# Kernel optimization log

Hardware: AMD Instinct MI355X
Metric: run time of the kernel (lower is better)

The kernel has to match this reference:

```python
import jax, jax.numpy as jnp
import numpy as np

FS = 5  # filter_size


def _extract_patches(x, fs):
    """x: (B, C, H, W) -> (B, C, fs*fs, H, W), 'same' padding, row-major
    shift order matching conv2d with an identity (one-hot) kernel."""
    B, C, H, W = x.shape
    pad = fs // 2
    xp = jnp.pad(x, ((0, 0), (0, 0), (pad, pad), (pad, pad)))
    shifts = [xp[:, :, i:i + H, j:j + W] for i in range(fs) for j in range(fs)]
    return jnp.stack(shifts, axis=2)


def setup_inputs() -> dict:
    key = jax.random.key(0)
    k1, k2 = jax.random.split(key)
    B, C, H, W = 8, 32, 128, 128
    x = jax.random.normal(k1, (B, C, H, W), dtype=jnp.float32)
    # PPDFGen modeled as a per-pixel linear map C -> fs^2 (1x1 conv) + bias
    w_gen = jax.random.normal(k2, (FS * FS, C), dtype=jnp.float32) * (1.0 / np.sqrt(C))
    b_gen = jnp.zeros((FS * FS,), dtype=jnp.float32)
    return {"x": x, "w_gen": w_gen, "b_gen": b_gen}


def reference(x, w_gen, b_gen):
    # Per-pixel dynamic filters: (B, fs^2, H, W)
    filters = jnp.einsum('bchw,fc->bfhw', x, w_gen) + b_gen[None, :, None, None]
    # Shifted patches (im2col via identity-kernel conv in the original):
    patches = _extract_patches(x, FS)            # (B, C, fs^2, H, W)
    # Elementwise multiply by filters (broadcast over channels) and reduce
    # over the fs^2 tap axis -- same math as the per-channel loop + concat.
    out = jnp.einsum('bcfhw,bfhw->bchw', patches, filters)
    return out
```

## Files before the change

### kernel.cpp

```cpp
#include <hip/hip_runtime.h>

#define FS    5
#define NTAP  25
#define Bc    8
#define Cc    32
#define Hc    128
#define Wc    128
#define HW    (Hc * Wc)

#define TH      8
#define TW      64
#define HALO_H  12
#define HALO_W  72
#define PLANE   (HALO_H * HALO_W)
#define LDS_FLOATS (Cc * PLANE)
#define LDS_BYTES  (LDS_FLOATS * 4)
#define F4_PER_PLANE (PLANE / 4)
#define F4_TOTAL     (Cc * F4_PER_PLANE)
#define INSTR_TOTAL  (F4_TOTAL / 64)
#define NWAVE        4
#define INSTR_PER_WAVE (INSTR_TOTAL / NWAVE)

__device__ __attribute__((aligned(16))) float ZERO4[4];

__device__ __forceinline__ void gload_lds16(const float* g, float* lds) {
    __builtin_amdgcn_global_load_lds(
        (const __attribute__((address_space(1))) void*)g,
        (__attribute__((address_space(3))) void*)lds, 16, 0, 0);
}

__global__ __launch_bounds__(256, 1) void ppdfn_fused(
    const float* __restrict__ x, const float* __restrict__ wg,
    const float* __restrict__ bg, float* __restrict__ out)
{
    extern __shared__ float xs[];

    const int tid  = threadIdx.x;
    const int lane = tid & 63;
    const int wv   = tid >> 6;
    const int ht   = blockIdx.x;
    const int wt   = blockIdx.y;
    const int b    = blockIdx.z;
    const int h0   = ht * TH;
    const int w0   = wt * TW;

    const float* xb = x + (size_t)b * Cc * HW;

    const int f_base = wv * (INSTR_PER_WAVE * 64) + lane;
#pragma unroll
    for (int k = 0; k < INSTR_PER_WAVE; ++k) {
        const int f  = f_base + k * 64;
        const int c  = f / F4_PER_PLANE;
        const int rm = f - c * F4_PER_PLANE;
        const int r  = rm / 18;
        const int c4 = rm - r * 18;
        const int gh = h0 - 2 + r;
        const int gw = w0 - 4 + 4 * c4;
        const bool v = ((unsigned)gh < (unsigned)Hc) &&
                       ((unsigned)gw <= (unsigned)(Wc - 4));
        const float* src = v ? (xb + (size_t)c * HW + gh * Wc + gw) : ZERO4;
        gload_lds16(src, xs + (size_t)(wv * INSTR_PER_WAVE + k) * 256);
    }
    asm volatile("s_waitcnt vmcnt(0)" ::: "memory");
    __syncthreads();

    const int ty = tid >> 5;
    const int tx = tid & 31;
    const int w2 = tx * 2;

    float fx[NTAP], fy[NTAP];
#pragma unroll
    for (int t = 0; t < NTAP; ++t) { const float bv = bg[t]; fx[t] = bv; fy[t] = bv; }

#pragma unroll 4
    for (int c = 0; c < Cc; ++c) {
        const float2 xv = *reinterpret_cast<const float2*>(
            xs + c * PLANE + (ty + 2) * HALO_W + (w2 + 4));
#pragma unroll
        for (int t = 0; t < NTAP; ++t) {
            const float wv_ = wg[t * Cc + c];
            fx[t] = fmaf(wv_, xv.x, fx[t]);
            fy[t] = fmaf(wv_, xv.y, fy[t]);
        }
    }

    float* ob = out + (size_t)b * Cc * HW + (h0 + ty) * Wc + (w0 + w2);
#pragma unroll 2
    for (int c = 0; c < Cc; ++c) {
        const float* p = xs + c * PLANE + ty * HALO_W + (w2 + 2);
        float ax = 0.f, ay = 0.f;
#pragma unroll
        for (int di = 0; di < FS; ++di) {
            const float* row = p + di * HALO_W;
            const float2 s01 = *reinterpret_cast<const float2*>(row);
            const float2 s23 = *reinterpret_cast<const float2*>(row + 2);
            const float2 s45 = *reinterpret_cast<const float2*>(row + 4);
            const float s0 = s01.x, s1 = s01.y, s2 = s23.x,
                        s3 = s23.y, s4 = s45.x, s5 = s45.y;
            ax = fmaf(fx[di * FS + 0], s0, ax);  ay = fmaf(fy[di * FS + 0], s1, ay);
            ax = fmaf(fx[di * FS + 1], s1, ax);  ay = fmaf(fy[di * FS + 1], s2, ay);
            ax = fmaf(fx[di * FS + 2], s2, ax);  ay = fmaf(fy[di * FS + 2], s3, ay);
            ax = fmaf(fx[di * FS + 3], s3, ax);  ay = fmaf(fy[di * FS + 3], s4, ay);
            ax = fmaf(fx[di * FS + 4], s4, ax);  ay = fmaf(fy[di * FS + 4], s5, ay);
        }
        *reinterpret_cast<float2*>(ob + (size_t)c * HW) = make_float2(ax, ay);
    }
}

extern "C" void kernel_launch(void* const* d_in, const int* in_sizes, int n_in,
                              void* d_out, int out_size, void* d_ws, size_t ws_size,
                              hipStream_t stream) {
    const float* x  = (const float*)d_in[0];
    const float* wg = (const float*)d_in[1];
    const float* bg = (const float*)d_in[2];
    float* out = (float*)d_out;

    ppdfn_fused<<<dim3(Hc / TH, Wc / TW, Bc), 256, LDS_BYTES, stream>>>(
        x, wg, bg, out);
}
```

Baseline: 23.24 us.

## Split channels across blocks, recomputing filters from directly loaded center pixels

Each block now handles only an 8-channel group, so it stages an 8-channel halo tile in LDS instead of all 32 channels. This cuts LDS per block and allows 4 blocks per CU, with 1024 blocks instead of 256. The per-pixel filters still need all 32 channels, so each block loads the other 24 channels' center pixels straight from global memory into registers, double-buffered to overlap with the FMAs. The cost is that filter generation is repeated four times per tile and there is extra global traffic for the center pixels.

```diff
diff --git a/kernel.cpp b/kernel.cpp
--- a/kernel.cpp
+++ b/kernel.cpp
@@ -4,6 +4,7 @@
 #define NTAP  25
 #define Bc    8
 #define Cc    32
+#define CG    8
 #define Hc    128
 #define Wc    128
 #define HW    (Hc * Wc)
@@ -13,13 +14,9 @@
 #define HALO_H  12
 #define HALO_W  72
 #define PLANE   (HALO_H * HALO_W)
-#define LDS_FLOATS (Cc * PLANE)
-#define LDS_BYTES  (LDS_FLOATS * 4)
 #define F4_PER_PLANE (PLANE / 4)
-#define F4_TOTAL     (Cc * F4_PER_PLANE)
-#define INSTR_TOTAL  (F4_TOTAL / 64)
-#define NWAVE        4
-#define INSTR_PER_WAVE (INSTR_TOTAL / NWAVE)
+#define F4_TOTAL     (CG * F4_PER_PLANE)
+#define LDS_BYTES    (CG * PLANE * 4)
 
 __device__ __attribute__((aligned(16))) float ZERO4[4];
 
@@ -29,64 +26,126 @@
         (__attribute__((address_space(3))) void*)lds, 16, 0, 0);
 }
 
-__global__ __launch_bounds__(256, 1) void ppdfn_fused(
+__global__ __launch_bounds__(256, 4) void ppdfn_fused(
     const float* __restrict__ x, const float* __restrict__ wg,
     const float* __restrict__ bg, float* __restrict__ out)
 {
     extern __shared__ float xs[];
 
-    const int tid  = threadIdx.x;
-    const int lane = tid & 63;
-    const int wv   = tid >> 6;
-    const int ht   = blockIdx.x;
-    const int wt   = blockIdx.y;
-    const int b    = blockIdx.z;
-    const int h0   = ht * TH;
-    const int w0   = wt * TW;
+    const int tid = threadIdx.x;
+    const int bid = blockIdx.x;
+    const int ht  = bid & 15;
+    const int wt  = (bid >> 4) & 1;
+    const int chg = (bid >> 5) & 3;
+    const int b   = bid >> 7;
+    const int h0  = ht * TH;
+    const int w0  = wt * TW;
+    const int c0  = chg * CG;
 
-    const float* xb = x + (size_t)b * Cc * HW;
+    const float* xb = x  + (size_t)b * Cc * HW;
+    const float* xo = xb + (size_t)c0 * HW;
 
-    const int f_base = wv * (INSTR_PER_WAVE * 64) + lane;
 #pragma unroll
-    for (int k = 0; k < INSTR_PER_WAVE; ++k) {
-        const int f  = f_base + k * 64;
-        const int c  = f / F4_PER_PLANE;
-        const int rm = f - c * F4_PER_PLANE;
-        const int r  = rm / 18;
-        const int c4 = rm - r * 18;
-        const int gh = h0 - 2 + r;
-        const int gw = w0 - 4 + 4 * c4;
-        const bool v = ((unsigned)gh < (unsigned)Hc) &&
-                       ((unsigned)gw <= (unsigned)(Wc - 4));
-        const float* src = v ? (xb + (size_t)c * HW + gh * Wc + gw) : ZERO4;
-        gload_lds16(src, xs + (size_t)(wv * INSTR_PER_WAVE + k) * 256);
+    for (int k = 0; k < 7; ++k) {
+        const int f = k * 256 + tid;
+        if (f < F4_TOTAL) {
+            const int c  = f / F4_PER_PLANE;
+            const int rm = f - c * F4_PER_PLANE;
+            const int r  = rm / 18;
+            const int c4 = rm - r * 18;
+            const int gh = h0 - 2 + r;
+            const int gw = w0 - 4 + 4 * c4;
+            const bool v = ((unsigned)gh < (unsigned)Hc) &&
+                           ((unsigned)gw <= (unsigned)(Wc - 4));
+            const float* src = v ? (xo + (size_t)c * HW + gh * Wc + gw) : ZERO4;
+            gload_lds16(src, xs + (size_t)k * 1024 + (size_t)(tid >> 6) * 256);
+        }
     }
-    asm volatile("s_waitcnt vmcnt(0)" ::: "memory");
-    __syncthreads();
 
     const int ty = tid >> 5;
     const int tx = tid & 31;
     const int w2 = tx * 2;
+    const int centerOff = (h0 + ty) * Wc + (w0 + w2);
+
+    const int og0 = ((chg + 1) & 3) * CG;
+    const int og1 = ((chg + 2) & 3) * CG;
+    const int og2 = ((chg + 3) & 3) * CG;
+
+    float2 xoA[CG], xoB[CG];
+    {
+        const float* p = xb + (size_t)og0 * HW + centerOff;
+#pragma unroll
+        for (int u = 0; u < CG; ++u)
+            xoA[u] = *reinterpret_cast<const float2*>(p + (size_t)u * HW);
+    }
 
     float fx[NTAP], fy[NTAP];
 #pragma unroll
     for (int t = 0; t < NTAP; ++t) { const float bv = bg[t]; fx[t] = bv; fy[t] = bv; }
 
-#pragma unroll 4
-    for (int c = 0; c < Cc; ++c) {
+    __syncthreads();
+
+#pragma unroll
+    for (int c = 0; c < CG; ++c) {
         const float2 xv = *reinterpret_cast<const float2*>(
             xs + c * PLANE + (ty + 2) * HALO_W + (w2 + 4));
+        const float* wrow = wg + (c0 + c);
 #pragma unroll
         for (int t = 0; t < NTAP; ++t) {
-            const float wv_ = wg[t * Cc + c];
-            fx[t] = fmaf(wv_, xv.x, fx[t]);
-            fy[t] = fmaf(wv_, xv.y, fy[t]);
+            const float wv = wrow[t * Cc];
+            fx[t] = fmaf(wv, xv.x, fx[t]);
+            fy[t] = fmaf(wv, xv.y, fy[t]);
+        }
+    }
+    {
+        const float* p = xb + (size_t)og1 * HW + centerOff;
+#pragma unroll
+        for (int u = 0; u < CG; ++u)
+            xoB[u] = *reinterpret_cast<const float2*>(p + (size_t)u * HW);
+    }
+#pragma unroll
+    for (int u = 0; u < CG; ++u) {
+        const float2 xv = xoA[u];
+        const float* wrow = wg + (og0 + u);
+#pragma unroll
+        for (int t = 0; t < NTAP; ++t) {
+            const float wv = wrow[t * Cc];
+            fx[t] = fmaf(wv, xv.x, fx[t]);
+            fy[t] = fmaf(wv, xv.y, fy[t]);
+        }
+    }
+    {
+        const float* p = xb + (size_t)og2 * HW + centerOff;
+#pragma unroll
+        for (int u = 0; u < CG; ++u)
+            xoA[u] = *reinterpret_cast<const float2*>(p + (size_t)u * HW);
+    }
+#pragma unroll
+    for (int u = 0; u < CG; ++u) {
+        const float2 xv = xoB[u];
+        const float* wrow = wg + (og1 + u);
+#pragma unroll
+        for (int t = 0; t < NTAP; ++t) {
+            const float wv = wrow[t * Cc];
+            fx[t] = fmaf(wv, xv.x, fx[t]);
+            fy[t] = fmaf(wv, xv.y, fy[t]);
+        }
+    }
+#pragma unroll
+    for (int u = 0; u < CG; ++u) {
+        const float2 xv = xoA[u];
+        const float* wrow = wg + (og2 + u);
+#pragma unroll
+        for (int t = 0; t < NTAP; ++t) {
+            const float wv = wrow[t * Cc];
+            fx[t] = fmaf(wv, xv.x, fx[t]);
+            fy[t] = fmaf(wv, xv.y, fy[t]);
         }
     }
 
-    float* ob = out + (size_t)b * Cc * HW + (h0 + ty) * Wc + (w0 + w2);
-#pragma unroll 2
-    for (int c = 0; c < Cc; ++c) {
+    float* ob = out + ((size_t)b * Cc + c0) * HW + centerOff;
+#pragma unroll
+    for (int c = 0; c < CG; ++c) {
         const float* p = xs + c * PLANE + ty * HALO_W + (w2 + 2);
         float ax = 0.f, ay = 0.f;
 #pragma unroll
@@ -115,6 +174,5 @@
     const float* bg = (const float*)d_in[2];
     float* out = (float*)d_out;
 
-    ppdfn_fused<<<dim3(Hc / TH, Wc / TW, Bc), 256, LDS_BYTES, stream>>>(
-        x, wg, bg, out);
+    ppdfn_fused<<<dim3(1024), 256, LDS_BYTES, stream>>>(x, wg, bg, out);
 }
```

Result: no change. 23.31 us (+0.3%).

## Split halo DMA waits to overlap filter computation with remaining loads

Applied to the files above, without the earlier changes.

Reorders the global-to-LDS DMA so each instruction index k covers the same region across all waves. Wait counts can then be split: the first 16 channels are consumed for filter generation while the second half is still in flight. The filter loop is restructured to cache 16 channel values in registers with tap-outer ordering, and the launch_bounds occupancy hint of 1 is dropped. This adds partial-wait complexity and relies on the vmcnt(13) count matching the per-thread load order.

```diff
diff --git a/kernel.cpp b/kernel.cpp
--- a/kernel.cpp
+++ b/kernel.cpp
@@ -2,7 +2,6 @@
 
 #define FS    5
 #define NTAP  25
-#define Bc    8
 #define Cc    32
 #define Hc    128
 #define Wc    128
@@ -13,13 +12,10 @@
 #define HALO_H  12
 #define HALO_W  72
 #define PLANE   (HALO_H * HALO_W)
-#define LDS_FLOATS (Cc * PLANE)
-#define LDS_BYTES  (LDS_FLOATS * 4)
 #define F4_PER_PLANE (PLANE / 4)
 #define F4_TOTAL     (Cc * F4_PER_PLANE)
-#define INSTR_TOTAL  (F4_TOTAL / 64)
-#define NWAVE        4
-#define INSTR_PER_WAVE (INSTR_TOTAL / NWAVE)
+#define DMA_PER_THREAD (F4_TOTAL / 256)
+#define LDS_BYTES (Cc * PLANE * 4)
 
 __device__ __attribute__((aligned(16))) float ZERO4[4];
 
@@ -29,27 +25,24 @@
         (__attribute__((address_space(3))) void*)lds, 16, 0, 0);
 }
 
-__global__ __launch_bounds__(256, 1) void ppdfn_fused(
+__global__ __launch_bounds__(256) void ppdfn_fused(
     const float* __restrict__ x, const float* __restrict__ wg,
     const float* __restrict__ bg, float* __restrict__ out)
 {
     extern __shared__ float xs[];
 
-    const int tid  = threadIdx.x;
-    const int lane = tid & 63;
-    const int wv   = tid >> 6;
-    const int ht   = blockIdx.x;
-    const int wt   = blockIdx.y;
-    const int b    = blockIdx.z;
-    const int h0   = ht * TH;
-    const int w0   = wt * TW;
+    const int tid = threadIdx.x;
+    const int ht  = blockIdx.x;
+    const int wt  = blockIdx.y;
+    const int b   = blockIdx.z;
+    const int h0  = ht * TH;
+    const int w0  = wt * TW;
 
     const float* xb = x + (size_t)b * Cc * HW;
 
-    const int f_base = wv * (INSTR_PER_WAVE * 64) + lane;
 #pragma unroll
-    for (int k = 0; k < INSTR_PER_WAVE; ++k) {
-        const int f  = f_base + k * 64;
+    for (int k = 0; k < DMA_PER_THREAD; ++k) {
+        const int f  = k * 256 + tid;
         const int c  = f / F4_PER_PLANE;
         const int rm = f - c * F4_PER_PLANE;
         const int r  = rm / 18;
@@ -59,10 +52,8 @@
         const bool v = ((unsigned)gh < (unsigned)Hc) &&
                        ((unsigned)gw <= (unsigned)(Wc - 4));
         const float* src = v ? (xb + (size_t)c * HW + gh * Wc + gw) : ZERO4;
-        gload_lds16(src, xs + (size_t)(wv * INSTR_PER_WAVE + k) * 256);
+        gload_lds16(src, xs + (size_t)k * 1024 + (size_t)(tid >> 6) * 256);
     }
-    asm volatile("s_waitcnt vmcnt(0)" ::: "memory");
-    __syncthreads();
 
     const int ty = tid >> 5;
     const int tx = tid & 31;
@@ -72,15 +63,42 @@
 #pragma unroll
     for (int t = 0; t < NTAP; ++t) { const float bv = bg[t]; fx[t] = bv; fy[t] = bv; }
 
-#pragma unroll 4
-    for (int c = 0; c < Cc; ++c) {
-        const float2 xv = *reinterpret_cast<const float2*>(
+    asm volatile("s_waitcnt vmcnt(13)" ::: "memory");
+    __builtin_amdgcn_sched_barrier(0);
+    __builtin_amdgcn_s_barrier();
+
+    float2 cv[16];
+#pragma unroll
+    for (int c = 0; c < 16; ++c)
+        cv[c] = *reinterpret_cast<const float2*>(
             xs + c * PLANE + (ty + 2) * HALO_W + (w2 + 4));
 #pragma unroll
-        for (int t = 0; t < NTAP; ++t) {
-            const float wv_ = wg[t * Cc + c];
-            fx[t] = fmaf(wv_, xv.x, fx[t]);
-            fy[t] = fmaf(wv_, xv.y, fy[t]);
+    for (int t = 0; t < NTAP; ++t) {
+        const float* wr = wg + t * Cc;
+#pragma unroll
+        for (int c = 0; c < 16; ++c) {
+            const float wv = wr[c];
+            fx[t] = fmaf(wv, cv[c].x, fx[t]);
+            fy[t] = fmaf(wv, cv[c].y, fy[t]);
+        }
+    }
+
+    asm volatile("s_waitcnt vmcnt(0)" ::: "memory");
+    __builtin_amdgcn_sched_barrier(0);
+    __builtin_amdgcn_s_barrier();
+
+#pragma unroll
+    for (int c = 0; c < 16; ++c)
+        cv[c] = *reinterpret_cast<const float2*>(
+            xs + (c + 16) * PLANE + (ty + 2) * HALO_W + (w2 + 4));
+#pragma unroll
+    for (int t = 0; t < NTAP; ++t) {
+        const float* wr = wg + t * Cc + 16;
+#pragma unroll
+        for (int c = 0; c < 16; ++c) {
+            const float wv = wr[c];
+            fx[t] = fmaf(wv, cv[c].x, fx[t]);
+            fy[t] = fmaf(wv, cv[c].y, fy[t]);
         }
     }
 
@@ -115,6 +133,6 @@
     const float* bg = (const float*)d_in[2];
     float* out = (float*)d_out;
 
-    ppdfn_fused<<<dim3(Hc / TH, Wc / TW, Bc), 256, LDS_BYTES, stream>>>(
+    ppdfn_fused<<<dim3(Hc / TH, Wc / TW, 8), 256, LDS_BYTES, stream>>>(
         x, wg, bg, out);
 }
```

After: 29.42 us. 26.6% more time.
